# Kernel tuning notes

Measured on AMD Instinct MI355X. Metric: run time of the kernel, lower is better.

Reference implementation:

```python
import jax, jax.numpy as jnp
import numpy as np

T = 16384   # sequence length (timesteps)
E = 1024    # embedding_size
H = 1024    # h_size == vocab (logits are the raw LSTM hidden output)


def setup_inputs() -> dict:
    key = jax.random.key(0)
    ks = jax.random.split(key, 6)
    s = 1.0 / np.sqrt(H)  # torch LSTM default init: U(-1/sqrt(H), 1/sqrt(H))
    Xs = jax.random.normal(ks[0], (T, E), jnp.float32)
    W_ih = jax.random.uniform(ks[1], (4 * H, E), jnp.float32, -s, s)
    W_hh = jax.random.uniform(ks[2], (4 * H, H), jnp.float32, -s, s)
    b_ih = jax.random.uniform(ks[3], (4 * H,), jnp.float32, -s, s)
    b_hh = jax.random.uniform(ks[4], (4 * H,), jnp.float32, -s, s)
    ys = jax.random.randint(ks[5], (T,), 0, H, dtype=jnp.int64)
    return {"Xs": Xs, "W_ih": W_ih, "W_hh": W_hh, "b_ih": b_ih, "b_hh": b_hh, "ys": ys}


def reference(Xs, W_ih, W_hh, b_ih, b_hh, ys):
    h_size = W_hh.shape[1]
    # input projections for all timesteps in one GEMM: [T, 4H]
    xg = Xs @ W_ih.T + b_ih + b_hh

    def step(carry, inp):
        h, c = carry
        xg_t, y_t = inp
        gates = xg_t + W_hh @ h  # [4H], torch gate order i,f,g,o
        i = jax.nn.sigmoid(gates[0 * h_size:1 * h_size])
        f = jax.nn.sigmoid(gates[1 * h_size:2 * h_size])
        g = jnp.tanh(gates[2 * h_size:3 * h_size])
        o = jax.nn.sigmoid(gates[3 * h_size:4 * h_size])
        c = f * c + i * g
        h = o * jnp.tanh(c)
        # cross-entropy on raw hidden output (vocab == h_size), batch 1
        loss_t = jax.nn.logsumexp(h) - h[y_t]
        return (h, c), loss_t

    h0 = jnp.zeros((h_size,), Xs.dtype)
    c0 = jnp.zeros((h_size,), Xs.dtype)
    (_, _), losses = jax.lax.scan(step, (h0, c0), (xg, ys))
    return jnp.sum(losses)
```

## Files before the change

### kernel.cpp

```cpp
#include <hip/hip_runtime.h>
#include <hip/hip_cooperative_groups.h>
#include <cstddef>

namespace cg = cooperative_groups;

#define T_STEPS 16384
#define E_DIM   1024
#define H_DIM   1024
#define G4      4096

#define NWG 128
#define NTH 512
#define EPW 8
#define CH  512
#define NCHUNK (T_STEPS / CH)
#define TKc 32

#define LDA(p)    __hip_atomic_load((p), __ATOMIC_RELAXED, __HIP_MEMORY_SCOPE_AGENT)
#define STA(p, v) __hip_atomic_store((p), (v), __ATOMIC_RELAXED, __HIP_MEMORY_SCOPE_AGENT)


__global__ __launch_bounds__(NTH) void lstm_fused_kernel(
    const float* __restrict__ Xs, const float* __restrict__ Wih,
    const float* __restrict__ Whh, const float* __restrict__ bih,
    const float* __restrict__ bhh, const int* __restrict__ ys,
    float* __restrict__ xgc,
    unsigned long long* __restrict__ hslot,
    float* __restrict__ partials,
    float* __restrict__ hy,
    float* __restrict__ wsum,
    float* __restrict__ out)
{
    cg::grid_group grid = cg::this_grid();
    const int w    = blockIdx.x;
    const int tid  = threadIdx.x;
    const int lane = tid & 63;
    const int j    = tid >> 6;
    const int gj   = w * EPW + j;

    __shared__ float hs[2][H_DIM];
    __shared__ float ered[16][EPW];
    __shared__ float red[8];
    __shared__ float As[TKc][68];
    __shared__ float Bs[TKc][132];

    float Wreg[4][16];
#pragma unroll
    for (int g = 0; g < 4; ++g) {
        const float* wr = Whh + (size_t)(g * H_DIM + gj) * H_DIM + lane;
#pragma unroll
        for (int m = 0; m < 16; ++m) Wreg[g][m] = wr[m << 6];
    }

    float c_state = 0.f;
    if (lane == 0) STA(&hslot[gj], 1ull << 32);

    const int nt   = w & 31;
    const int n0   = nt * 128;
    const int tx4  = (tid & 31) * 4;
    const int ty4  = (tid >> 5) * 4;
    const int lrow = tid >> 3;
    const int lkg  = (tid & 7) * 4;

    float4 bias_v;
    {
        const float4 bi = *(const float4*)&bih[n0 + tx4];
        const float4 bh = *(const float4*)&bhh[n0 + tx4];
        bias_v.x = bi.x + bh.x; bias_v.y = bi.y + bh.y;
        bias_v.z = bi.z + bh.z; bias_v.w = bi.w + bh.w;
    }

    const float gate_scale = (lane == 2) ? 2.f : 1.f;
    const float gate_mul   = (lane == 2) ? 2.f : 1.f;
    const float gate_add   = (lane == 2) ? -1.f : 0.f;

    float xv = 0.f;
    int   yt = 0;

    for (int c = 0; c < NCHUNK; ++c) {
        const int t0 = c * CH;

#pragma unroll
        for (int rep = 0; rep < 2; ++rep) {
            const int mt = (w >> 5) + rep * 4;
            float acc[4][4];
#pragma unroll
            for (int i = 0; i < 4; ++i)
#pragma unroll
                for (int jj = 0; jj < 4; ++jj) acc[i][jj] = 0.f;

            const float* Arow = Xs + (size_t)(t0 + mt * 64 + lrow) * E_DIM + lkg;

            for (int kc = 0; kc < E_DIM; kc += TKc) {
                __syncthreads();
                float4 av = *(const float4*)(Arow + kc);
                As[lkg + 0][lrow] = av.x; As[lkg + 1][lrow] = av.y;
                As[lkg + 2][lrow] = av.z; As[lkg + 3][lrow] = av.w;
#pragma unroll
                for (int r2 = 0; r2 < 2; ++r2) {
                    int br = r2 * 64 + lrow;
                    float4 bv = *(const float4*)&Wih[(size_t)(n0 + br) * E_DIM + kc + lkg];
                    Bs[lkg + 0][br] = bv.x; Bs[lkg + 1][br] = bv.y;
                    Bs[lkg + 2][br] = bv.z; Bs[lkg + 3][br] = bv.w;
                }
                __syncthreads();
#pragma unroll
                for (int kk = 0; kk < TKc; ++kk) {
                    float4 a = *(const float4*)&As[kk][ty4];
                    float4 b = *(const float4*)&Bs[kk][tx4];
                    acc[0][0] = fmaf(a.x, b.x, acc[0][0]); acc[0][1] = fmaf(a.x, b.y, acc[0][1]);
                    acc[0][2] = fmaf(a.x, b.z, acc[0][2]); acc[0][3] = fmaf(a.x, b.w, acc[0][3]);
                    acc[1][0] = fmaf(a.y, b.x, acc[1][0]); acc[1][1] = fmaf(a.y, b.y, acc[1][1]);
                    acc[1][2] = fmaf(a.y, b.z, acc[1][2]); acc[1][3] = fmaf(a.y, b.w, acc[1][3]);
                    acc[2][0] = fmaf(a.z, b.x, acc[2][0]); acc[2][1] = fmaf(a.z, b.y, acc[2][1]);
                    acc[2][2] = fmaf(a.z, b.z, acc[2][2]); acc[2][3] = fmaf(a.z, b.w, acc[2][3]);
                    acc[3][0] = fmaf(a.w, b.x, acc[3][0]); acc[3][1] = fmaf(a.w, b.y, acc[3][1]);
                    acc[3][2] = fmaf(a.w, b.z, acc[3][2]); acc[3][3] = fmaf(a.w, b.w, acc[3][3]);
                }
            }
#pragma unroll
            for (int i = 0; i < 4; ++i) {
                int lr = mt * 64 + ty4 + i;
                float4 ov;
                ov.x = acc[i][0] + bias_v.x; ov.y = acc[i][1] + bias_v.y;
                ov.z = acc[i][2] + bias_v.z; ov.w = acc[i][3] + bias_v.w;
                *(float4*)&xgc[(size_t)lr * G4 + n0 + tx4] = ov;
            }
        }
        __threadfence();
        grid.sync();

        if (lane < 4) xv = xgc[lane * H_DIM + gj];

        for (int lt = 0; lt < CH; ++lt) {
            const int t = t0 + lt;
            const int p = t & 1;

            if (lane == 0) yt = ys[t];

            {
                const unsigned htag = (unsigned)(t + 1);
                const unsigned long long* hp =
                    hslot + ((size_t)(t & 3) << 10) + 2 * tid;
                unsigned long long v0, v1;
                do {
                    v0 = LDA(hp);
                    v1 = LDA(hp + 1);
                } while ((unsigned)(v0 >> 32) != htag || (unsigned)(v1 >> 32) != htag);
                hs[p][2 * tid]     = __uint_as_float((unsigned)v0);
                hs[p][2 * tid + 1] = __uint_as_float((unsigned)v1);
            }
            __syncthreads();

            if ((t & 7) == 0 && t >= 8 && j == ((t >> 3) & 7)) {
                const int b = t - 8;
                float e = ered[(b & 15) + (lane >> 3)][lane & 7];
                e += __shfl_xor(e, 1);
                e += __shfl_xor(e, 2);
                e += __shfl_xor(e, 4);
                if ((lane & 7) == 0)
                    partials[(size_t)w * T_STEPS + b + (lane >> 3)] = e;
            }

            float xn = 0.f;
            if (lane < 4 && lt + 1 < CH)
                xn = xgc[(size_t)(lt + 1) * G4 + lane * H_DIM + gj];

            float a0 = 0.f, a1 = 0.f, a2 = 0.f, a3 = 0.f;
#pragma unroll
            for (int m = 0; m < 16; ++m) {
                float hvv = hs[p][lane + (m << 6)];
                a0 = fmaf(Wreg[0][m], hvv, a0);
                a1 = fmaf(Wreg[1][m], hvv, a1);
                a2 = fmaf(Wreg[2][m], hvv, a2);
                a3 = fmaf(Wreg[3][m], hvv, a3);
            }
#pragma unroll
            for (int off = 32; off >= 1; off >>= 1) {
                a0 += __shfl_xor(a0, off);
                a1 += __shfl_xor(a1, off);
                a2 += __shfl_xor(a2, off);
                a3 += __shfl_xor(a3, off);
            }

            float sel = (lane == 1) ? a1 : (lane == 2) ? a2 : (lane == 3) ? a3 : a0;
            float x   = sel + xv;
            float sg  = 1.f / (1.f + __expf(-gate_scale * x));
            float act = fmaf(sg, gate_mul, gate_add);

            float ii = act;
            float ff = __shfl(act, 1);
            float gg = __shfl(act, 2);
            float oo = __shfl(act, 3);
            c_state  = fmaf(ff, c_state, ii * gg);
            float tc = 2.f / (1.f + __expf(-2.f * c_state)) - 1.f;
            float h  = oo * tc;

            if (lane == 0) {
                STA(&hslot[((size_t)((t + 1) & 3) << 10) + gj],
                    ((unsigned long long)(unsigned)(t + 2) << 32) |
                    (unsigned long long)__float_as_uint(h));
                ered[t & 15][j] = __expf(h);
                if (gj == yt) hy[t] = h;
            }
            xv = xn;
        }
    }

    __syncthreads();
    if (j == 0) {
        const int b = T_STEPS - 8;
        float e = ered[(b & 15) + (lane >> 3)][lane & 7];
        e += __shfl_xor(e, 1);
        e += __shfl_xor(e, 2);
        e += __shfl_xor(e, 4);
        if ((lane & 7) == 0)
            partials[(size_t)w * T_STEPS + b + (lane >> 3)] = e;
    }
    __threadfence();
    grid.sync();

    if (w < 32) {
        int t = w * NTH + tid;
        float s = 0.f;
        for (int i = 0; i < NWG; ++i) s += partials[(size_t)i * T_STEPS + t];
        float val = logf(s) - hy[t];
#pragma unroll
        for (int off = 32; off >= 1; off >>= 1) val += __shfl_xor(val, off);
        if (lane == 0) red[tid >> 6] = val;
        __syncthreads();
        if (tid == 0) {
            float s2 = 0.f;
#pragma unroll
            for (int i = 0; i < 8; ++i) s2 += red[i];
            wsum[w] = s2;
        }
    }
    __threadfence();
    grid.sync();
    if (w == 0 && tid == 0) {
        float s = 0.f;
        for (int i = 0; i < 32; ++i) s += wsum[i];
        out[0] = s;
    }
}

extern "C" void kernel_launch(void* const* d_in, const int* in_sizes, int n_in,
                              void* d_out, int out_size, void* d_ws, size_t ws_size,
                              hipStream_t stream)
{
    const float* Xs  = (const float*)d_in[0];
    const float* Wih = (const float*)d_in[1];
    const float* Whh = (const float*)d_in[2];
    const float* bih = (const float*)d_in[3];
    const float* bhh = (const float*)d_in[4];
    const int*   ys  = (const int*)d_in[5];

    float* xgc                = (float*)d_ws;
    unsigned long long* hslot = (unsigned long long*)(xgc + (size_t)CH * G4);
    float* partials           = (float*)(hslot + 4 * H_DIM);
    float* hy                 = partials + (size_t)NWG * T_STEPS;
    float* wsum               = hy + T_STEPS;
    float* out                = (float*)d_out;

    void* args[] = {(void*)&Xs, (void*)&Wih, (void*)&Whh, (void*)&bih, (void*)&bhh,
                    (void*)&ys, (void*)&xgc, (void*)&hslot, (void*)&partials,
                    (void*)&hy, (void*)&wsum, (void*)&out};
    hipLaunchCooperativeKernel((void*)lstm_fused_kernel,
                               dim3(NWG), dim3(NTH), args, 0, stream);
}
```

Baseline: 36.10 ms.

## Split workgroups into recurrent and input-GEMM producers with tagged double buffer

Launches 256 workgroups: 128 run the sequential LSTM recurrence and 128 compute the input-projection GEMM chunk by chunk into a double-buffered workspace. Each value is tagged with its chunk number, so recurrent lanes spin on the tag instead of waiting at a grid-wide barrier before every chunk. Producers throttle themselves by polling the h-slot step tags so they never overwrite a buffer still in use. This takes the GEMM and the per-chunk grid syncs off the serial critical path, at the cost of doubling workspace traffic with 64-bit tagged stores and relying on 256 co-resident workgroups plus spin-wait correctness.

```diff
diff --git a/kernel.cpp b/kernel.cpp
--- a/kernel.cpp
+++ b/kernel.cpp
@@ -9,22 +9,24 @@
 #define H_DIM   1024
 #define G4      4096
 
-#define NWG 128
-#define NTH 512
-#define EPW 8
-#define CH  512
+#define NRWG 128
+#define NGWG 128
+#define NTOT (NRWG + NGWG)
+#define NTH  512
+#define EPW  8
+#define CH   256
 #define NCHUNK (T_STEPS / CH)
-#define TKc 32
+#define TKc  32
 
 #define LDA(p)    __hip_atomic_load((p), __ATOMIC_RELAXED, __HIP_MEMORY_SCOPE_AGENT)
 #define STA(p, v) __hip_atomic_store((p), (v), __ATOMIC_RELAXED, __HIP_MEMORY_SCOPE_AGENT)
 
 
-__global__ __launch_bounds__(NTH) void lstm_fused_kernel(
+__global__ __launch_bounds__(NTH) void lstm_split2_kernel(
     const float* __restrict__ Xs, const float* __restrict__ Wih,
     const float* __restrict__ Whh, const float* __restrict__ bih,
     const float* __restrict__ bhh, const int* __restrict__ ys,
-    float* __restrict__ xgc,
+    unsigned long long* __restrict__ xg2,
     unsigned long long* __restrict__ hslot,
     float* __restrict__ partials,
     float* __restrict__ hy,
@@ -32,11 +34,10 @@
     float* __restrict__ out)
 {
     cg::grid_group grid = cg::this_grid();
-    const int w    = blockIdx.x;
+    const int blk  = blockIdx.x;
     const int tid  = threadIdx.x;
     const int lane = tid & 63;
     const int j    = tid >> 6;
-    const int gj   = w * EPW + j;
 
     __shared__ float hs[2][H_DIM];
     __shared__ float ered[16][EPW];
@@ -44,52 +45,203 @@
     __shared__ float As[TKc][68];
     __shared__ float Bs[TKc][132];
 
-    float Wreg[4][16];
-#pragma unroll
-    for (int g = 0; g < 4; ++g) {
-        const float* wr = Whh + (size_t)(g * H_DIM + gj) * H_DIM + lane;
-#pragma unroll
-        for (int m = 0; m < 16; ++m) Wreg[g][m] = wr[m << 6];
-    }
-
-    float c_state = 0.f;
-    if (lane == 0) STA(&hslot[gj], 1ull << 32);
-
-    const int nt   = w & 31;
-    const int n0   = nt * 128;
-    const int tx4  = (tid & 31) * 4;
-    const int ty4  = (tid >> 5) * 4;
-    const int lrow = tid >> 3;
-    const int lkg  = (tid & 7) * 4;
-
-    float4 bias_v;
-    {
-        const float4 bi = *(const float4*)&bih[n0 + tx4];
-        const float4 bh = *(const float4*)&bhh[n0 + tx4];
-        bias_v.x = bi.x + bh.x; bias_v.y = bi.y + bh.y;
-        bias_v.z = bi.z + bh.z; bias_v.w = bi.w + bh.w;
-    }
-
-    const float gate_scale = (lane == 2) ? 2.f : 1.f;
-    const float gate_mul   = (lane == 2) ? 2.f : 1.f;
-    const float gate_add   = (lane == 2) ? -1.f : 0.f;
-
-    float xv = 0.f;
-    int   yt = 0;
-
-    for (int c = 0; c < NCHUNK; ++c) {
-        const int t0 = c * CH;
-
-#pragma unroll
-        for (int rep = 0; rep < 2; ++rep) {
-            const int mt = (w >> 5) + rep * 4;
+    if (blk < NRWG) {
+        const int w  = blk;
+        const int gj = w * EPW + j;
+
+        float Wreg[4][16];
+#pragma unroll
+        for (int g = 0; g < 4; ++g) {
+            const float* wr = Whh + (size_t)(g * H_DIM + gj) * H_DIM + lane;
+#pragma unroll
+            for (int m = 0; m < 16; ++m) Wreg[g][m] = wr[m << 6];
+        }
+
+        float c_state = 0.f;
+        if (lane == 0) STA(&hslot[gj], 1ull << 32);
+
+        const float gate_scale = (lane == 2) ? 2.f : 1.f;
+        const float gate_mul   = (lane == 2) ? 2.f : 1.f;
+        const float gate_add   = (lane == 2) ? -1.f : 0.f;
+
+        unsigned long long xe = 0;
+        if (lane < 4) xe = LDA(&xg2[(size_t)lane * H_DIM + gj]);
+        int yt = 0;
+        if (lane == 2) yt = ys[0];
+
+        for (int t = 0; t < T_STEPS; ++t) {
+            const int p = t & 1;
+
+            {
+                const unsigned htag = (unsigned)(t + 1);
+                const unsigned long long* hp =
+                    hslot + ((size_t)(t & 3) << 10) + 2 * tid;
+                unsigned long long v0, v1;
+                do {
+                    v0 = LDA(hp);
+                    v1 = LDA(hp + 1);
+                } while ((unsigned)(v0 >> 32) != htag || (unsigned)(v1 >> 32) != htag);
+                hs[p][2 * tid]     = __uint_as_float((unsigned)v0);
+                hs[p][2 * tid + 1] = __uint_as_float((unsigned)v1);
+            }
+            __syncthreads();
+
+            if ((t & 7) == 0 && t >= 8 && j == ((t >> 3) & 7)) {
+                const int b = t - 8;
+                float e = ered[(b & 15) + (lane >> 3)][lane & 7];
+                e += __shfl_xor(e, 1);
+                e += __shfl_xor(e, 2);
+                e += __shfl_xor(e, 4);
+                if ((lane & 7) == 0)
+                    partials[(size_t)w * T_STEPS + b + (lane >> 3)] = e;
+            }
+
+            float xvv = 0.f;
+            if (lane < 4) {
+                const unsigned ctag = (unsigned)((t >> 8) + 1);
+                const unsigned long long* px = xg2 +
+                    ((size_t)((t >> 8) & 1) * CH + (t & (CH - 1))) * G4 +
+                    (size_t)lane * H_DIM + gj;
+                unsigned long long e = xe;
+                while ((unsigned)(e >> 32) != ctag) e = LDA(px);
+                xvv = __uint_as_float((unsigned)e);
+            }
+            if (lane < 4 && t + 1 < T_STEPS) {
+                const int tn = t + 1;
+                xe = LDA(xg2 +
+                         ((size_t)((tn >> 8) & 1) * CH + (tn & (CH - 1))) * G4 +
+                         (size_t)lane * H_DIM + gj);
+            }
+
+            float a0 = 0.f, a1 = 0.f, a2 = 0.f, a3 = 0.f;
+#pragma unroll
+            for (int m = 0; m < 16; ++m) {
+                float hvv = hs[p][lane + (m << 6)];
+                a0 = fmaf(Wreg[0][m], hvv, a0);
+                a1 = fmaf(Wreg[1][m], hvv, a1);
+                a2 = fmaf(Wreg[2][m], hvv, a2);
+                a3 = fmaf(Wreg[3][m], hvv, a3);
+            }
+#pragma unroll
+            for (int off = 32; off >= 1; off >>= 1) {
+                a0 += __shfl_xor(a0, off);
+                a1 += __shfl_xor(a1, off);
+                a2 += __shfl_xor(a2, off);
+                a3 += __shfl_xor(a3, off);
+            }
+
+            float sel = (lane == 1) ? a1 : (lane == 2) ? a2 : (lane == 3) ? a3 : a0;
+            float x   = sel + xvv;
+            float sg  = 1.f / (1.f + __expf(-gate_scale * x));
+            float act = fmaf(sg, gate_mul, gate_add);
+
+            float ii = __shfl(act, 0);
+            float ff = __shfl(act, 1);
+            float gg = __shfl(act, 2);
+            float oo = __shfl(act, 3);
+            c_state  = fmaf(ff, c_state, ii * gg);
+            float tc = 2.f / (1.f + __expf(-2.f * c_state)) - 1.f;
+            float h  = oo * tc;
+
+            if (lane == 0) {
+                STA(&hslot[((size_t)((t + 1) & 3) << 10) + gj],
+                    ((unsigned long long)(unsigned)(t + 2) << 32) |
+                    (unsigned long long)__float_as_uint(h));
+            }
+            if (lane == 1) ered[t & 15][j] = __expf(h);
+            if (lane == 2) {
+                if (gj == yt) hy[t] = h;
+                yt = ys[(t + 1 < T_STEPS) ? t + 1 : 0];
+            }
+        }
+
+        __syncthreads();
+        if (j == 0) {
+            const int b = T_STEPS - 8;
+            float e = ered[(b & 15) + (lane >> 3)][lane & 7];
+            e += __shfl_xor(e, 1);
+            e += __shfl_xor(e, 2);
+            e += __shfl_xor(e, 4);
+            if ((lane & 7) == 0)
+                partials[(size_t)w * T_STEPS + b + (lane >> 3)] = e;
+        }
+        __threadfence();
+        grid.sync();
+
+        if (w < 32) {
+            int t = w * NTH + tid;
+            float s = 0.f;
+            for (int i = 0; i < NRWG; ++i) s += partials[(size_t)i * T_STEPS + t];
+            float val = logf(s) - hy[t];
+#pragma unroll
+            for (int off = 32; off >= 1; off >>= 1) val += __shfl_xor(val, off);
+            if (lane == 0) red[tid >> 6] = val;
+            __syncthreads();
+            if (tid == 0) {
+                float s2 = 0.f;
+#pragma unroll
+                for (int i = 0; i < 8; ++i) s2 += red[i];
+                wsum[w] = s2;
+            }
+        }
+        __threadfence();
+        grid.sync();
+        if (blk == 0 && tid == 0) {
+            float s = 0.f;
+            for (int i = 0; i < 32; ++i) s += wsum[i];
+            out[0] = s;
+        }
+    } else {
+        const int wq   = blk - NRWG;
+        const int mt   = wq >> 5;
+        const int nt   = wq & 31;
+        const int n0   = nt * 128;
+        const int tx4  = (tid & 31) * 4;
+        const int ty4  = (tid >> 5) * 4;
+        const int lrow = tid >> 3;
+        const int lkg  = (tid & 7) * 4;
+
+        float4 bias_v;
+        {
+            const float4 bi = *(const float4*)&bih[n0 + tx4];
+            const float4 bh = *(const float4*)&bhh[n0 + tx4];
+            bias_v.x = bi.x + bh.x; bias_v.y = bi.y + bh.y;
+            bias_v.z = bi.z + bh.z; bias_v.w = bi.w + bh.w;
+        }
+
+        for (int c = 0; c < NCHUNK; ++c) {
+            if (c >= 2) {
+                if (tid == 0) {
+                    if (c == 2) {
+                        for (;;) {
+                            unsigned long long v = LDA(&hslot[0]);
+                            if ((unsigned)(v >> 32) < 1000u) break;
+                            __builtin_amdgcn_s_sleep(32);
+                        }
+                    }
+                    const unsigned thr = (unsigned)((c - 1) * CH + 3);
+                    for (;;) {
+                        unsigned best = 0;
+#pragma unroll
+                        for (int s = 0; s < 4; ++s) {
+                            unsigned long long v = LDA(&hslot[(size_t)s << 10]);
+                            unsigned tg = (unsigned)(v >> 32);
+                            if (tg <= (unsigned)(T_STEPS + 2) && tg > best) best = tg;
+                        }
+                        if (best >= thr) break;
+                        __builtin_amdgcn_s_sleep(32);
+                    }
+                }
+                __syncthreads();
+            }
+
             float acc[4][4];
 #pragma unroll
             for (int i = 0; i < 4; ++i)
 #pragma unroll
                 for (int jj = 0; jj < 4; ++jj) acc[i][jj] = 0.f;
 
-            const float* Arow = Xs + (size_t)(t0 + mt * 64 + lrow) * E_DIM + lkg;
+            const float* Arow = Xs + (size_t)(c * CH + mt * 64 + lrow) * E_DIM + lkg;
 
             for (int kc = 0; kc < E_DIM; kc += TKc) {
                 __syncthreads();
@@ -118,130 +270,25 @@
                     acc[3][2] = fmaf(a.w, b.z, acc[3][2]); acc[3][3] = fmaf(a.w, b.w, acc[3][3]);
                 }
             }
+
+            unsigned long long* xb = xg2 + (size_t)(c & 1) * CH * G4;
+            const unsigned long long tg = (unsigned long long)(unsigned)(c + 1) << 32;
 #pragma unroll
             for (int i = 0; i < 4; ++i) {
                 int lr = mt * 64 + ty4 + i;
-                float4 ov;
-                ov.x = acc[i][0] + bias_v.x; ov.y = acc[i][1] + bias_v.y;
-                ov.z = acc[i][2] + bias_v.z; ov.w = acc[i][3] + bias_v.w;
-                *(float4*)&xgc[(size_t)lr * G4 + n0 + tx4] = ov;
-            }
-        }
-        __threadfence();
+                size_t base = (size_t)lr * G4 + n0 + tx4;
+                float o0 = acc[i][0] + bias_v.x;
+                float o1 = acc[i][1] + bias_v.y;
+                float o2 = acc[i][2] + bias_v.z;
+                float o3 = acc[i][3] + bias_v.w;
+                STA(&xb[base + 0], tg | (unsigned long long)__float_as_uint(o0));
+                STA(&xb[base + 1], tg | (unsigned long long)__float_as_uint(o1));
+                STA(&xb[base + 2], tg | (unsigned long long)__float_as_uint(o2));
+                STA(&xb[base + 3], tg | (unsigned long long)__float_as_uint(o3));
+            }
+        }
         grid.sync();
-
-        if (lane < 4) xv = xgc[lane * H_DIM + gj];
-
-        for (int lt = 0; lt < CH; ++lt) {
-            const int t = t0 + lt;
-            const int p = t & 1;
-
-            if (lane == 0) yt = ys[t];
-
-            {
-                const unsigned htag = (unsigned)(t + 1);
-                const unsigned long long* hp =
-                    hslot + ((size_t)(t & 3) << 10) + 2 * tid;
-                unsigned long long v0, v1;
-                do {
-                    v0 = LDA(hp);
-                    v1 = LDA(hp + 1);
-                } while ((unsigned)(v0 >> 32) != htag || (unsigned)(v1 >> 32) != htag);
-                hs[p][2 * tid]     = __uint_as_float((unsigned)v0);
-                hs[p][2 * tid + 1] = __uint_as_float((unsigned)v1);
-            }
-            __syncthreads();
-
-            if ((t & 7) == 0 && t >= 8 && j == ((t >> 3) & 7)) {
-                const int b = t - 8;
-                float e = ered[(b & 15) + (lane >> 3)][lane & 7];
-                e += __shfl_xor(e, 1);
-                e += __shfl_xor(e, 2);
-                e += __shfl_xor(e, 4);
-                if ((lane & 7) == 0)
-                    partials[(size_t)w * T_STEPS + b + (lane >> 3)] = e;
-            }
-
-            float xn = 0.f;
-            if (lane < 4 && lt + 1 < CH)
-                xn = xgc[(size_t)(lt + 1) * G4 + lane * H_DIM + gj];
-
-            float a0 = 0.f, a1 = 0.f, a2 = 0.f, a3 = 0.f;
-#pragma unroll
-            for (int m = 0; m < 16; ++m) {
-                float hvv = hs[p][lane + (m << 6)];
-                a0 = fmaf(Wreg[0][m], hvv, a0);
-                a1 = fmaf(Wreg[1][m], hvv, a1);
-                a2 = fmaf(Wreg[2][m], hvv, a2);
-                a3 = fmaf(Wreg[3][m], hvv, a3);
-            }
-#pragma unroll
-            for (int off = 32; off >= 1; off >>= 1) {
-                a0 += __shfl_xor(a0, off);
-                a1 += __shfl_xor(a1, off);
-                a2 += __shfl_xor(a2, off);
-                a3 += __shfl_xor(a3, off);
-            }
-
-            float sel = (lane == 1) ? a1 : (lane == 2) ? a2 : (lane == 3) ? a3 : a0;
-            float x   = sel + xv;
-            float sg  = 1.f / (1.f + __expf(-gate_scale * x));
-            float act = fmaf(sg, gate_mul, gate_add);
-
-            float ii = act;
-            float ff = __shfl(act, 1);
-            float gg = __shfl(act, 2);
-            float oo = __shfl(act, 3);
-            c_state  = fmaf(ff, c_state, ii * gg);
-            float tc = 2.f / (1.f + __expf(-2.f * c_state)) - 1.f;
-            float h  = oo * tc;
-
-            if (lane == 0) {
-                STA(&hslot[((size_t)((t + 1) & 3) << 10) + gj],
-                    ((unsigned long long)(unsigned)(t + 2) << 32) |
-                    (unsigned long long)__float_as_uint(h));
-                ered[t & 15][j] = __expf(h);
-                if (gj == yt) hy[t] = h;
-            }
-            xv = xn;
-        }
-    }
-
-    __syncthreads();
-    if (j == 0) {
-        const int b = T_STEPS - 8;
-        float e = ered[(b & 15) + (lane >> 3)][lane & 7];
-        e += __shfl_xor(e, 1);
-        e += __shfl_xor(e, 2);
-        e += __shfl_xor(e, 4);
-        if ((lane & 7) == 0)
-            partials[(size_t)w * T_STEPS + b + (lane >> 3)] = e;
-    }
-    __threadfence();
-    grid.sync();
-
-    if (w < 32) {
-        int t = w * NTH + tid;
-        float s = 0.f;
-        for (int i = 0; i < NWG; ++i) s += partials[(size_t)i * T_STEPS + t];
-        float val = logf(s) - hy[t];
-#pragma unroll
-        for (int off = 32; off >= 1; off >>= 1) val += __shfl_xor(val, off);
-        if (lane == 0) red[tid >> 6] = val;
-        __syncthreads();
-        if (tid == 0) {
-            float s2 = 0.f;
-#pragma unroll
-            for (int i = 0; i < 8; ++i) s2 += red[i];
-            wsum[w] = s2;
-        }
-    }
-    __threadfence();
-    grid.sync();
-    if (w == 0 && tid == 0) {
-        float s = 0.f;
-        for (int i = 0; i < 32; ++i) s += wsum[i];
-        out[0] = s;
+        grid.sync();
     }
 }
 
@@ -256,16 +303,16 @@
     const float* bhh = (const float*)d_in[4];
     const int*   ys  = (const int*)d_in[5];
 
-    float* xgc                = (float*)d_ws;
-    unsigned long long* hslot = (unsigned long long*)(xgc + (size_t)CH * G4);
+    unsigned long long* xg2   = (unsigned long long*)d_ws;
+    unsigned long long* hslot = xg2 + (size_t)2 * CH * G4;
     float* partials           = (float*)(hslot + 4 * H_DIM);
-    float* hy                 = partials + (size_t)NWG * T_STEPS;
+    float* hy                 = partials + (size_t)NRWG * T_STEPS;
     float* wsum               = hy + T_STEPS;
     float* out                = (float*)d_out;
 
     void* args[] = {(void*)&Xs, (void*)&Wih, (void*)&Whh, (void*)&bih, (void*)&bhh,
-                    (void*)&ys, (void*)&xgc, (void*)&hslot, (void*)&partials,
+                    (void*)&ys, (void*)&xg2, (void*)&hslot, (void*)&partials,
                     (void*)&hy, (void*)&wsum, (void*)&out};
-    hipLaunchCooperativeKernel((void*)lstm_fused_kernel,
-                               dim3(NWG), dim3(NTH), args, 0, stream);
+    hipLaunchCooperativeKernel((void*)lstm_split2_kernel,
+                               dim3(NTOT), dim3(NTH), args, 0, stream);
 }
```

Measured after the change: 60.61 ms. 67.9% more time.
